# Kernel tuning notes

Hardware: AMD Instinct MI355X
Metric: run time of the kernel (lower is better)

## Reference

```python
import jax, jax.numpy as jnp
import numpy as np

NUM_BANDS, B, K, D = 5, 512, 64, 200
H = 4            # num attention heads
HID = 512        # selector hidden width
S = 0.02         # weight init scale


def setup_inputs() -> dict:
    key = jax.random.key(0)
    ks = jax.random.split(key, 8)
    F_IN = NUM_BANDS * K * D  # 64000
    return {
        "bands": jax.random.normal(ks[0], (NUM_BANDS, B, K, D), jnp.float32),
        "w1": jax.random.normal(ks[1], (HID, F_IN), jnp.float32) * S,
        "b1": jnp.zeros((HID,), jnp.float32),
        "w2": jax.random.normal(ks[2], (NUM_BANDS, HID), jnp.float32) * S,
        "b2": jnp.zeros((NUM_BANDS,), jnp.float32),
        "in_proj_w": jax.random.normal(ks[3], (3 * D, D), jnp.float32) * S,
        "in_proj_b": jnp.zeros((3 * D,), jnp.float32),
        "out_w": jax.random.normal(ks[4], (D, D), jnp.float32) * S,
        "out_b": jnp.zeros((D,), jnp.float32),
    }


def reference(bands, w1, b1, w2, b2, in_proj_w, in_proj_b, out_w, out_b):
    nb, Bb, k, d = bands.shape
    hd = d // H
    scale = 1.0 / np.sqrt(hd)

    # concat(bands, dim=1): [B, nb*k, d] in band-major order
    x = jnp.transpose(bands, (1, 0, 2, 3))           # [B, nb, k, d]
    kv_in = x.reshape(Bb, nb * k, d)                 # [B, nb*k, d]

    # router MLP + softmax + argmax band select
    flat = kv_in.reshape(Bb, -1)                     # [B, nb*k*d]
    h = jax.nn.relu(flat @ w1.T + b1)                # [B, HID]
    band_weights = jax.nn.softmax(h @ w2.T + b2, axis=-1)
    sel = jnp.argmax(band_weights, axis=-1)          # [B] int

    # gather selected band per sample as the query
    Q = bands[sel, jnp.arange(Bb)]                   # [B, k, d]

    # multihead cross-attention (torch nn.MultiheadAttention math)
    wq, wk, wv = jnp.split(in_proj_w, 3, axis=0)
    bq, bk, bv = jnp.split(in_proj_b, 3, axis=0)
    q = (Q @ wq.T + bq).reshape(Bb, k, H, hd).transpose(0, 2, 1, 3)        # [B,H,k,hd]
    kk = (kv_in @ wk.T + bk).reshape(Bb, nb * k, H, hd).transpose(0, 2, 1, 3)
    v = (kv_in @ wv.T + bv).reshape(Bb, nb * k, H, hd).transpose(0, 2, 1, 3)

    attn = jax.nn.softmax(jnp.einsum('bhqe,bhke->bhqk', q, kk) * scale, axis=-1)
    o = jnp.einsum('bhqk,bhke->bhqe', attn, v)       # [B,H,k,hd]
    o = o.transpose(0, 2, 1, 3).reshape(Bb, k, d)
    return o @ out_w.T + out_b                        # [B, k, d]
```

## Files before the change

### kernel.cpp

```cpp
#include <hip/hip_runtime.h>
#include <hip/hip_bf16.h>

#define NBANDS 5
#define BATCH  512
#define KQN    64
#define DM     200
#define NHEAD  4
#define HD     50
#define HIDW   512
#define TKV    320
#define FIN    64000
#define KSPLIT 20
#define KCH    3200
#define RCH    50
#define KPAD   232
#define NTT    13
#define KST    7
#define PLANE_ELEMS (KST * NTT * 64 * 8)

typedef __bf16  bf16x8 __attribute__((ext_vector_type(8)));
typedef float   f32x4  __attribute__((ext_vector_type(4)));

static __device__ inline unsigned short f2bf(float f) {
    __hip_bfloat16 h = __float2bfloat16(f);
    return *reinterpret_cast<unsigned short*>(&h);
}
static __device__ inline float bf2f(unsigned short u) {
    union { unsigned int i; float f; } x;
    x.i = ((unsigned int)u) << 16;
    return x.f;
}
static __device__ inline bf16x8 bf8zero() {
    union { bf16x8 v; unsigned int u[4]; } z;
    z.u[0] = z.u[1] = z.u[2] = z.u[3] = 0u;
    return z.v;
}
static __device__ inline void split8(const float4& a, const float4& b,
                                     bf16x8& hi, bf16x8& lo) {
    union { bf16x8 v; unsigned short u[8]; } H, L;
    const float xs[8] = {a.x, a.y, a.z, a.w, b.x, b.y, b.z, b.w};
#pragma unroll
    for (int i = 0; i < 8; ++i) {
        H.u[i] = f2bf(xs[i]);
        L.u[i] = f2bf(xs[i] - bf2f(H.u[i]));
    }
    hi = H.v; lo = L.v;
}

__global__ __launch_bounds__(256) void k_router_mfma(
    const float* __restrict__ bands, const float* __restrict__ w1,
    float* __restrict__ part)
{
    __shared__ __align__(16) unsigned short Ah[64][72];
    __shared__ __align__(16) unsigned short Al[64][72];
    __shared__ __align__(16) unsigned short Bh[64][72];
    __shared__ __align__(16) unsigned short Bl[64][72];

    const int lin     = (blockIdx.z << 6) + (blockIdx.y << 3) + blockIdx.x;
    const int logical = (lin & 7) * 160 + (lin >> 3);
    const int z   = logical >> 6;
    const int rem = logical & 63;
    const int j0  = (rem & 7) << 6;
    const int b0  = (rem >> 3) << 6;

    const int t  = threadIdx.x;
    const int w  = t >> 6, lane = t & 63;
    const int lm = lane & 15, quad = lane >> 4;
    const int m0 = w * 16;

    const int row0 = t >> 4, c4 = (t & 15) * 4;

    f32x4 acc[4];
#pragma unroll
    for (int nt = 0; nt < 4; ++nt) acc[nt] = (f32x4){0.f, 0.f, 0.f, 0.f};

    const int kbase = z * KCH;
    for (int chunk = 0; chunk < RCH; ++chunk) {
        const int kc = kbase + chunk * 64;
        const int band = kc / 12800;
        const float* abase = bands + (size_t)band * 6540800 + kc + c4;
        const float* bbase = w1 + (size_t)j0 * FIN + kc + c4;
        float4 av[4], bv[4];
#pragma unroll
        for (int r = 0; r < 4; ++r)
            av[r] = *(const float4*)(abase + (size_t)(b0 + row0 + r * 16) * 12800);
#pragma unroll
        for (int r = 0; r < 4; ++r)
            bv[r] = *(const float4*)(bbase + (size_t)(row0 + r * 16) * FIN);
        __syncthreads();
#pragma unroll
        for (int r = 0; r < 4; ++r) {
            const int row = row0 + r * 16;
            ushort4 hh, ll;
            hh.x = f2bf(av[r].x); ll.x = f2bf(av[r].x - bf2f(hh.x));
            hh.y = f2bf(av[r].y); ll.y = f2bf(av[r].y - bf2f(hh.y));
            hh.z = f2bf(av[r].z); ll.z = f2bf(av[r].z - bf2f(hh.z));
            hh.w = f2bf(av[r].w); ll.w = f2bf(av[r].w - bf2f(hh.w));
            *(ushort4*)&Ah[row][c4] = hh;
            *(ushort4*)&Al[row][c4] = ll;
        }
#pragma unroll
        for (int r = 0; r < 4; ++r) {
            const int row = row0 + r * 16;
            ushort4 hh, ll;
            hh.x = f2bf(bv[r].x); ll.x = f2bf(bv[r].x - bf2f(hh.x));
            hh.y = f2bf(bv[r].y); ll.y = f2bf(bv[r].y - bf2f(hh.y));
            hh.z = f2bf(bv[r].z); ll.z = f2bf(bv[r].z - bf2f(hh.z));
            hh.w = f2bf(bv[r].w); ll.w = f2bf(bv[r].w - bf2f(hh.w));
            *(ushort4*)&Bh[row][c4] = hh;
            *(ushort4*)&Bl[row][c4] = ll;
        }
        __syncthreads();
#pragma unroll
        for (int ks = 0; ks < 2; ++ks) {
            const int ka = ks * 32 + quad * 8;
            const bf16x8 a_h = *(const bf16x8*)&Ah[m0 + lm][ka];
            const bf16x8 a_l = *(const bf16x8*)&Al[m0 + lm][ka];
#pragma unroll
            for (int nt = 0; nt < 4; ++nt) {
                const bf16x8 b_h = *(const bf16x8*)&Bh[nt * 16 + lm][ka];
                const bf16x8 b_l = *(const bf16x8*)&Bl[nt * 16 + lm][ka];
                acc[nt] = __builtin_amdgcn_mfma_f32_16x16x32_bf16(a_h, b_h, acc[nt], 0, 0, 0);
                acc[nt] = __builtin_amdgcn_mfma_f32_16x16x32_bf16(a_l, b_h, acc[nt], 0, 0, 0);
                acc[nt] = __builtin_amdgcn_mfma_f32_16x16x32_bf16(a_h, b_l, acc[nt], 0, 0, 0);
            }
        }
    }
    float* po = part + (size_t)z * (BATCH * HIDW);
#pragma unroll
    for (int nt = 0; nt < 4; ++nt) {
        const int jj = j0 + nt * 16 + lm;
#pragma unroll
        for (int reg = 0; reg < 4; ++reg) {
            const int bb = b0 + m0 + quad * 4 + reg;
            po[(size_t)bb * HIDW + jj] = acc[nt][reg];
        }
    }
}

__global__ __launch_bounds__(256) void k_reduce_relu(
    const float* __restrict__ part, const float* __restrict__ b1,
    float* __restrict__ h)
{
    const int tid = blockIdx.x * 256 + threadIdx.x;
    float s = b1[tid & (HIDW - 1)];
#pragma unroll
    for (int z = 0; z < KSPLIT; ++z) s += part[z * (BATCH * HIDW) + tid];
    h[tid] = fmaxf(s, 0.f);
}

__global__ __launch_bounds__(256) void k_wprep(
    const float* __restrict__ ipw, unsigned short* __restrict__ Wb)
{
    const int j = blockIdx.x;
    const int c = threadIdx.x;
    if (c < KPAD) {
        const float v = (c < DM) ? ipw[(size_t)(DM + j) * DM + c] : 0.f;
        Wb[(size_t)j * KPAD + c] = f2bf(v);
    }
}

__global__ __launch_bounds__(256) void k_wpack(
    const float* __restrict__ ipw, const float* __restrict__ outw,
    unsigned short* __restrict__ WqHp, unsigned short* __restrict__ WqLp,
    unsigned short* __restrict__ OwHp, unsigned short* __restrict__ OwLp)
{
    const int p = blockIdx.x;
    const int ks = p / NTT, nt = p - ks * NTT;
    const int t = threadIdx.x;
    const int lane = t >> 2, e0 = (t & 3) * 2;
    const int lm = lane & 15, quad = lane >> 4;
    const int row = nt * 16 + lm;
    const int k  = ks * 32 + quad * 8 + e0;
    const float* src = (blockIdx.y == 0) ? ipw : outw;
    unsigned short* dh = (blockIdx.y == 0) ? WqHp : OwHp;
    unsigned short* dl = (blockIdx.y == 0) ? WqLp : OwLp;
    float v0 = 0.f, v1 = 0.f;
    if (row < DM && k < DM) {
        v0 = src[(size_t)row * DM + k];
        v1 = src[(size_t)row * DM + k + 1];
    }
    const int off = (p << 9) + (lane << 3) + e0;
    const unsigned short h0 = f2bf(v0), h1 = f2bf(v1);
    dh[off]     = h0;
    dh[off + 1] = h1;
    dl[off]     = f2bf(v0 - bf2f(h0));
    dl[off + 1] = f2bf(v1 - bf2f(h1));
}

__global__ __launch_bounds__(256) void k_argmax(
    const float* __restrict__ h, const float* __restrict__ w2,
    const float* __restrict__ b2, int* __restrict__ sel)
{
    __shared__ float red[NBANDS][256];
    const int b = blockIdx.x, t = threadIdx.x;
    float acc[NBANDS] = {0.f, 0.f, 0.f, 0.f, 0.f};
    for (int j = t; j < HIDW; j += 256) {
        const float hv = h[b * HIDW + j];
#pragma unroll
        for (int n = 0; n < NBANDS; ++n)
            acc[n] = fmaf(hv, w2[n * HIDW + j], acc[n]);
    }
#pragma unroll
    for (int n = 0; n < NBANDS; ++n) red[n][t] = acc[n];
    __syncthreads();
    for (int s = 128; s > 0; s >>= 1) {
        if (t < s) {
#pragma unroll
            for (int n = 0; n < NBANDS; ++n) red[n][t] += red[n][t + s];
        }
        __syncthreads();
    }
    if (t == 0) {
        int best = 0;
        float bv = red[0][0] + b2[0];
        for (int n = 1; n < NBANDS; ++n) {
            const float v = red[n][0] + b2[n];
            if (v > bv) { bv = v; best = n; }
        }
        sel[b] = best;
    }
}

template<bool BF16OUT>
static __device__ inline void proj_core(
    const float* __restrict__ x0,
    const unsigned short* __restrict__ Ph,
    const unsigned short* __restrict__ Pl,
    const float* __restrict__ bias,
    void* __restrict__ outp)
{
    const int t = threadIdx.x;
    const int w = t >> 6, lane = t & 63;
    const int lm = lane & 15, quad = lane >> 4;
    const int m0 = w * 16;
    const float* xrow = x0 + (size_t)(m0 + lm) * DM;

    f32x4 acc[NTT];
#pragma unroll
    for (int nt = 0; nt < NTT; ++nt) acc[nt] = (f32x4){0.f, 0.f, 0.f, 0.f};

#pragma unroll
    for (int ks = 0; ks < KST; ++ks) {
        const int k0 = ks * 32 + quad * 8;
        bf16x8 a_h = bf8zero(), a_l = bf8zero();
        if (k0 + 8 <= DM) {
            const float4 xa = *(const float4*)(xrow + k0);
            const float4 xb = *(const float4*)(xrow + k0 + 4);
            split8(xa, xb, a_h, a_l);
        }
        const unsigned short* ph = Ph + ((ks * NTT) << 9) + (lane << 3);
        const unsigned short* pl = Pl + ((ks * NTT) << 9) + (lane << 3);
#pragma unroll
        for (int nt = 0; nt < NTT; ++nt) {
            const bf16x8 b_h = *(const bf16x8*)(ph + (nt << 9));
            const bf16x8 b_l = *(const bf16x8*)(pl + (nt << 9));
            acc[nt] = __builtin_amdgcn_mfma_f32_16x16x32_bf16(a_h, b_h, acc[nt], 0, 0, 0);
            acc[nt] = __builtin_amdgcn_mfma_f32_16x16x32_bf16(a_l, b_h, acc[nt], 0, 0, 0);
            acc[nt] = __builtin_amdgcn_mfma_f32_16x16x32_bf16(a_h, b_l, acc[nt], 0, 0, 0);
        }
    }
#pragma unroll
    for (int nt = 0; nt < NTT; ++nt) {
        const int col = nt * 16 + lm;
        if (col < DM) {
            const float bs = bias[col];
#pragma unroll
            for (int reg = 0; reg < 4; ++reg) {
                const int row = m0 + quad * 4 + reg;
                const float v = acc[nt][reg] + bs;
                if (BF16OUT)
                    ((unsigned short*)outp)[(size_t)row * DM + col] = f2bf(v);
                else
                    ((float*)outp)[(size_t)row * DM + col] = v;
            }
        }
    }
}

__global__ __launch_bounds__(256) void k_qproj_mfma(
    const float* __restrict__ bands, const int* __restrict__ sel,
    const unsigned short* __restrict__ WqHp, const unsigned short* __restrict__ WqLp,
    const float* __restrict__ ipb, unsigned short* __restrict__ qb)
{
    const int b = blockIdx.x;
    const int band = sel[b];
    const float* x0 = bands + (size_t)((band * BATCH + b) * KQN) * DM;
    proj_core<true>(x0, WqHp, WqLp, ipb, qb + (size_t)(b * KQN) * DM);
}

__global__ __launch_bounds__(256) void k_outproj_mfma(
    const float* __restrict__ obuf, const unsigned short* __restrict__ OwHp,
    const unsigned short* __restrict__ OwLp, const float* __restrict__ outb,
    float* __restrict__ out)
{
    const int b = blockIdx.x;
    proj_core<false>(obuf + (size_t)(b * KQN) * DM, OwHp, OwLp, outb,
                     out + (size_t)(b * KQN) * DM);
}

__global__ __launch_bounds__(256) void k_kvproj(
    const float* __restrict__ bands, const unsigned short* __restrict__ Wb,
    const float* __restrict__ ipb, __hip_bfloat16* __restrict__ Kp,
    __hip_bfloat16* __restrict__ Vp)
{
    __shared__ __align__(16) unsigned short Xs[64][KPAD];
    __shared__ __align__(16) unsigned short Ws[80][KPAD];
    __shared__ float Bbias[80];
    const int t  = threadIdx.x;
    const int M0 = blockIdx.x * 64;
    const int n0 = blockIdx.y * 80;

    {
        const float4* wsrc = (const float4*)(Wb + (size_t)n0 * KPAD);
        float4* wdst = (float4*)&Ws[0][0];
        for (int i = t; i < 2320; i += 256) wdst[i] = wsrc[i];
    }
    if (t < 80) Bbias[t] = ipb[DM + n0 + t];
    for (int i = t; i < 64 * 50; i += 256) {
        const int r = i / 50, g = i - r * 50;
        const int gg = M0 + r;
        const int bb = gg / TKV, tk = gg - bb * TKV;
        const int band = tk >> 6, kk = tk & 63;
        const float4 x4 = *(const float4*)(bands
            + ((size_t)((band * BATCH + bb) * KQN + kk)) * DM + g * 4);
        ushort4 u;
        u.x = f2bf(x4.x); u.y = f2bf(x4.y); u.z = f2bf(x4.z); u.w = f2bf(x4.w);
        *(ushort4*)&Xs[r][g * 4] = u;
    }
    for (int i = t; i < 64 * 8; i += 256) {
        const int r = i >> 3, g = i & 7;
        ushort4 z; z.x = 0; z.y = 0; z.z = 0; z.w = 0;
        *(ushort4*)&Xs[r][DM + g * 4] = z;
    }
    __syncthreads();

    const int w = t >> 6, lane = t & 63;
    const int lm = lane & 15, quad = lane >> 4;
    const int m0 = w * 16;
    f32x4 acc[5];
#pragma unroll
    for (int nt = 0; nt < 5; ++nt) acc[nt] = (f32x4){0.f, 0.f, 0.f, 0.f};

#pragma unroll
    for (int ks = 0; ks < 7; ++ks) {
        const int ka = ks * 32 + quad * 8;
        const bf16x8 a = *(const bf16x8*)&Xs[m0 + lm][ka];
#pragma unroll
        for (int nt = 0; nt < 5; ++nt) {
            const bf16x8 bb8 = *(const bf16x8*)&Ws[nt * 16 + lm][ka];
            acc[nt] = __builtin_amdgcn_mfma_f32_16x16x32_bf16(a, bb8, acc[nt], 0, 0, 0);
        }
    }
#pragma unroll
    for (int nt = 0; nt < 5; ++nt) {
        const int col = n0 + nt * 16 + lm;
        const float bias = Bbias[nt * 16 + lm];
#pragma unroll
        for (int reg = 0; reg < 4; ++reg) {
            const int grow = M0 + m0 + quad * 4 + reg;
            const float v = acc[nt][reg] + bias;
            if (col < DM) Kp[(size_t)grow * DM + col] = __float2bfloat16(v);
            else          Vp[(size_t)grow * DM + (col - DM)] = __float2bfloat16(v);
        }
    }
}

__global__ __launch_bounds__(256) void k_attn(
    const unsigned short* __restrict__ qb, const __hip_bfloat16* __restrict__ Kp,
    const __hip_bfloat16* __restrict__ Vp, float* __restrict__ obuf)
{
    __shared__ __align__(16) unsigned short Qs[64][72];
    __shared__ __align__(16) unsigned short KP[320][72];
    __shared__ __align__(16) unsigned short Vt[64][328];
    __shared__ __align__(16) unsigned short Ps[64][328];
    const int b = blockIdx.x, hh = blockIdx.y;
    const int t = threadIdx.x;

    const unsigned short* qbase = qb + (size_t)(b * KQN) * DM + hh * HD;
    for (int idx = t; idx < 64 * 64; idx += 256) {
        const int r = idx >> 6, e = idx & 63;
        Qs[r][e] = (e < HD) ? qbase[(size_t)r * DM + e] : 0;
    }
    const unsigned short* kbase = (const unsigned short*)Kp + (size_t)b * TKV * DM + hh * HD;
    for (int idx = t; idx < 320 * 25; idx += 256) {
        const int key = idx / 25, g = idx - key * 25;
        *(unsigned int*)&KP[key][g * 2] =
            *(const unsigned int*)(kbase + (size_t)key * DM + g * 2);
    }
    for (int idx = t; idx < 320 * 7; idx += 256) {
        const int key = idx / 7, g = idx - key * 7;
        *(unsigned int*)&KP[key][50 + g * 2] = 0;
    }
    const unsigned short* vbase = (const unsigned short*)Vp + (size_t)b * TKV * DM + hh * HD;
    for (int idx = t; idx < 320 * 25; idx += 256) {
        const int key = idx / 25, g = idx - key * 25;
        const unsigned int v = *(const unsigned int*)(vbase + (size_t)key * DM + g * 2);
        Vt[g * 2][key]     = (unsigned short)(v & 0xffffu);
        Vt[g * 2 + 1][key] = (unsigned short)(v >> 16);
    }
    __syncthreads();

    const int w = t >> 6, lane = t & 63;
    const int lm = lane & 15, quad = lane >> 4;
    const int m0 = w * 16;

    f32x4 s[20];
#pragma unroll
    for (int nt = 0; nt < 20; ++nt) s[nt] = (f32x4){0.f, 0.f, 0.f, 0.f};
#pragma unroll
    for (int ks = 0; ks < 2; ++ks) {
        const int ka = ks * 32 + quad * 8;
        const bf16x8 a = *(const bf16x8*)&Qs[m0 + lm][ka];
#pragma unroll
        for (int nt = 0; nt < 20; ++nt) {
            const bf16x8 bb8 = *(const bf16x8*)&KP[nt * 16 + lm][ka];
            s[nt] = __builtin_amdgcn_mfma_f32_16x16x32_bf16(a, bb8, s[nt], 0, 0, 0);
        }
    }

    const float scale = 0.14142135623730951f;
    float inv[4];
#pragma unroll
    for (int reg = 0; reg < 4; ++reg) {
        float mx = -1e30f;
#pragma unroll
        for (int nt = 0; nt < 20; ++nt) {
            const float sv = s[nt][reg] * scale;
            s[nt][reg] = sv;
            mx = fmaxf(mx, sv);
        }
#pragma unroll
        for (int off = 1; off < 16; off <<= 1)
            mx = fmaxf(mx, __shfl_xor(mx, off, 64));
        float lsum = 0.f;
#pragma unroll
        for (int nt = 0; nt < 20; ++nt) {
            const float p = __expf(s[nt][reg] - mx);
            s[nt][reg] = p;
            lsum += p;
        }
#pragma unroll
        for (int off = 1; off < 16; off <<= 1)
            lsum += __shfl_xor(lsum, off, 64);
        inv[reg] = 1.f / lsum;
    }
#pragma unroll
    for (int reg = 0; reg < 4; ++reg) {
        const int row = m0 + quad * 4 + reg;
#pragma unroll
        for (int nt = 0; nt < 20; ++nt)
            Ps[row][nt * 16 + lm] = f2bf(s[nt][reg]);
    }
    __syncthreads();

    f32x4 o[4];
#pragma unroll
    for (int nt = 0; nt < 4; ++nt) o[nt] = (f32x4){0.f, 0.f, 0.f, 0.f};
#pragma unroll
    for (int ks = 0; ks < 10; ++ks) {
        const int ka = ks * 32 + quad * 8;
        const bf16x8 a = *(const bf16x8*)&Ps[m0 + lm][ka];
#pragma unroll
        for (int nt = 0; nt < 4; ++nt) {
            const bf16x8 bb8 = *(const bf16x8*)&Vt[nt * 16 + lm][ka];
            o[nt] = __builtin_amdgcn_mfma_f32_16x16x32_bf16(a, bb8, o[nt], 0, 0, 0);
        }
    }
    float* op = obuf + (size_t)(b * KQN) * DM + hh * HD;
#pragma unroll
    for (int nt = 0; nt < 4; ++nt) {
        const int e = nt * 16 + lm;
        if (e < HD) {
#pragma unroll
            for (int reg = 0; reg < 4; ++reg) {
                const int row = m0 + quad * 4 + reg;
                op[(size_t)row * DM + e] = o[nt][reg] * inv[reg];
            }
        }
    }
}

extern "C" void kernel_launch(void* const* d_in, const int* in_sizes, int n_in,
                              void* d_out, int out_size, void* d_ws, size_t ws_size,
                              hipStream_t stream)
{
    const float* bands = (const float*)d_in[0];
    const float* w1    = (const float*)d_in[1];
    const float* b1    = (const float*)d_in[2];
    const float* w2    = (const float*)d_in[3];
    const float* b2    = (const float*)d_in[4];
    const float* ipw   = (const float*)d_in[5];
    const float* ipb   = (const float*)d_in[6];
    const float* outw  = (const float*)d_in[7];
    const float* outb  = (const float*)d_in[8];
    float* out = (float*)d_out;

    if (ws_size < (size_t)192940032) return;

    char* ws = (char*)d_ws;
    int*   sel  = (int*)  (ws + 0);
    float* part = (float*)(ws + 4096);
    float* h    = (float*)(ws + 20975616);
    unsigned short* qb = (unsigned short*)(ws + 4096);
    unsigned short* Wb = (unsigned short*)(ws + 26218496);
    unsigned short* WqHp = (unsigned short*)(ws + 26404096);
    unsigned short* WqLp = (unsigned short*)(ws + 26497280);
    unsigned short* OwHp = (unsigned short*)(ws + 26590464);
    unsigned short* OwLp = (unsigned short*)(ws + 26683648);
    __hip_bfloat16* Kp = (__hip_bfloat16*)(ws + 26776832);
    __hip_bfloat16* Vp = (__hip_bfloat16*)(ws + 92312832);
    float* obuf = (float*)(ws + 157848832);

    k_wprep<<<400, 256, 0, stream>>>(ipw, Wb);
    k_wpack<<<dim3(KST * NTT, 2), 256, 0, stream>>>(ipw, outw, WqHp, WqLp, OwHp, OwLp);

    k_router_mfma<<<dim3(8, 8, KSPLIT), 256, 0, stream>>>(bands, w1, part);
    k_reduce_relu<<<(BATCH * HIDW) / 256, 256, 0, stream>>>(part, b1, h);
    k_argmax<<<BATCH, 256, 0, stream>>>(h, w2, b2, sel);
    k_qproj_mfma<<<BATCH, 256, 0, stream>>>(bands, sel, WqHp, WqLp, ipb, qb);
    k_kvproj<<<dim3(2560, 5), 256, 0, stream>>>(bands, Wb, ipb, Kp, Vp);
    k_attn<<<dim3(BATCH, NHEAD), 256, 0, stream>>>(qb, Kp, Vp, obuf);
    k_outproj_mfma<<<BATCH, 256, 0, stream>>>(obuf, OwHp, OwLp, outb, out);
}
```

Before: 935.7 us.

## Fuse K/V projection column tiles and feed MFMA from pre-packed global weights

The K/V projection kernel previously launched 5 column blocks per row tile, each re-reading and re-converting the same bands rows into LDS. It now computes all 400 K/V columns per block (25 accumulator tiles), loading each activation row straight from global into registers once. Weights are pre-packed into MFMA fragment order so they can be read directly from global/L2 without LDS staging or syncs. This cuts redundant reads of bands, at the cost of much higher register pressure (100 accumulator floats) and uncached global weight fetches per MFMA.

Result: no change. 941.9 us (+0.7%).

```diff
diff --git a/kernel.cpp b/kernel.cpp
--- a/kernel.cpp
+++ b/kernel.cpp
@@ -13,9 +13,9 @@
 #define KSPLIT 20
 #define KCH    3200
 #define RCH    50
-#define KPAD   232
 #define NTT    13
 #define KST    7
+#define NTKV   25
 #define PLANE_ELEMS (KST * NTT * 64 * 8)
 
 typedef __bf16  bf16x8 __attribute__((ext_vector_type(8)));
@@ -45,6 +45,13 @@
         L.u[i] = f2bf(xs[i] - bf2f(H.u[i]));
     }
     hi = H.v; lo = L.v;
+}
+static __device__ inline bf16x8 round8(const float4& a, const float4& b) {
+    union { bf16x8 v; unsigned short u[8]; } H;
+    const float xs[8] = {a.x, a.y, a.z, a.w, b.x, b.y, b.z, b.w};
+#pragma unroll
+    for (int i = 0; i < 8; ++i) H.u[i] = f2bf(xs[i]);
+    return H.v;
 }
 
 __global__ __launch_bounds__(256) void k_router_mfma(
@@ -147,17 +154,6 @@
 #pragma unroll
     for (int z = 0; z < KSPLIT; ++z) s += part[z * (BATCH * HIDW) + tid];
     h[tid] = fmaxf(s, 0.f);
-}
-
-__global__ __launch_bounds__(256) void k_wprep(
-    const float* __restrict__ ipw, unsigned short* __restrict__ Wb)
-{
-    const int j = blockIdx.x;
-    const int c = threadIdx.x;
-    if (c < KPAD) {
-        const float v = (c < DM) ? ipw[(size_t)(DM + j) * DM + c] : 0.f;
-        Wb[(size_t)j * KPAD + c] = f2bf(v);
-    }
 }
 
 __global__ __launch_bounds__(256) void k_wpack(
@@ -188,6 +184,26 @@
     dl[off + 1] = f2bf(v1 - bf2f(h1));
 }
 
+__global__ __launch_bounds__(256) void k_wpack_kv(
+    const float* __restrict__ ipw, unsigned short* __restrict__ Wkv)
+{
+    const int p = blockIdx.x;
+    const int ks = p / NTKV, nt = p - ks * NTKV;
+    const int t = threadIdx.x;
+    const int lane = t >> 2, e0 = (t & 3) * 2;
+    const int lm = lane & 15, quad = lane >> 4;
+    const int row = nt * 16 + lm;
+    const int k  = ks * 32 + quad * 8 + e0;
+    float v0 = 0.f, v1 = 0.f;
+    if (k < DM) {
+        v0 = ipw[(size_t)(DM + row) * DM + k];
+        v1 = ipw[(size_t)(DM + row) * DM + k + 1];
+    }
+    const int off = (p << 9) + (lane << 3) + e0;
+    Wkv[off]     = f2bf(v0);
+    Wkv[off + 1] = f2bf(v1);
+}
+
 __global__ __launch_bounds__(256) void k_argmax(
     const float* __restrict__ h, const float* __restrict__ w2,
     const float* __restrict__ b2, int* __restrict__ sel)
@@ -299,63 +315,46 @@
                      out + (size_t)(b * KQN) * DM);
 }
 
-__global__ __launch_bounds__(256) void k_kvproj(
-    const float* __restrict__ bands, const unsigned short* __restrict__ Wb,
+__global__ __launch_bounds__(256) void k_kvproj_pk(
+    const float* __restrict__ bands, const unsigned short* __restrict__ Wkv,
     const float* __restrict__ ipb, __hip_bfloat16* __restrict__ Kp,
     __hip_bfloat16* __restrict__ Vp)
 {
-    __shared__ __align__(16) unsigned short Xs[64][KPAD];
-    __shared__ __align__(16) unsigned short Ws[80][KPAD];
-    __shared__ float Bbias[80];
-    const int t  = threadIdx.x;
-    const int M0 = blockIdx.x * 64;
-    const int n0 = blockIdx.y * 80;
-
-    {
-        const float4* wsrc = (const float4*)(Wb + (size_t)n0 * KPAD);
-        float4* wdst = (float4*)&Ws[0][0];
-        for (int i = t; i < 2320; i += 256) wdst[i] = wsrc[i];
-    }
-    if (t < 80) Bbias[t] = ipb[DM + n0 + t];
-    for (int i = t; i < 64 * 50; i += 256) {
-        const int r = i / 50, g = i - r * 50;
-        const int gg = M0 + r;
-        const int bb = gg / TKV, tk = gg - bb * TKV;
-        const int band = tk >> 6, kk = tk & 63;
-        const float4 x4 = *(const float4*)(bands
-            + ((size_t)((band * BATCH + bb) * KQN + kk)) * DM + g * 4);
-        ushort4 u;
-        u.x = f2bf(x4.x); u.y = f2bf(x4.y); u.z = f2bf(x4.z); u.w = f2bf(x4.w);
-        *(ushort4*)&Xs[r][g * 4] = u;
-    }
-    for (int i = t; i < 64 * 8; i += 256) {
-        const int r = i >> 3, g = i & 7;
-        ushort4 z; z.x = 0; z.y = 0; z.z = 0; z.w = 0;
-        *(ushort4*)&Xs[r][DM + g * 4] = z;
-    }
-    __syncthreads();
-
+    const int t = threadIdx.x;
     const int w = t >> 6, lane = t & 63;
     const int lm = lane & 15, quad = lane >> 4;
     const int m0 = w * 16;
-    f32x4 acc[5];
-#pragma unroll
-    for (int nt = 0; nt < 5; ++nt) acc[nt] = (f32x4){0.f, 0.f, 0.f, 0.f};
-
-#pragma unroll
-    for (int ks = 0; ks < 7; ++ks) {
-        const int ka = ks * 32 + quad * 8;
-        const bf16x8 a = *(const bf16x8*)&Xs[m0 + lm][ka];
-#pragma unroll
-        for (int nt = 0; nt < 5; ++nt) {
-            const bf16x8 bb8 = *(const bf16x8*)&Ws[nt * 16 + lm][ka];
-            acc[nt] = __builtin_amdgcn_mfma_f32_16x16x32_bf16(a, bb8, acc[nt], 0, 0, 0);
-        }
-    }
-#pragma unroll
-    for (int nt = 0; nt < 5; ++nt) {
-        const int col = n0 + nt * 16 + lm;
-        const float bias = Bbias[nt * 16 + lm];
+    const int M0 = blockIdx.x * 64;
+
+    const int gg = M0 + m0 + lm;
+    const int bb = gg / TKV, tk = gg - bb * TKV;
+    const int band = tk >> 6, kk = tk & 63;
+    const float* xrow = bands + (size_t)((band * BATCH + bb) * KQN + kk) * DM;
+
+    f32x4 acc[NTKV];
+#pragma unroll
+    for (int nt = 0; nt < NTKV; ++nt) acc[nt] = (f32x4){0.f, 0.f, 0.f, 0.f};
+
+#pragma unroll
+    for (int ks = 0; ks < KST; ++ks) {
+        const int k0 = ks * 32 + quad * 8;
+        bf16x8 a = bf8zero();
+        if (k0 + 8 <= DM) {
+            const float4 xa = *(const float4*)(xrow + k0);
+            const float4 xb = *(const float4*)(xrow + k0 + 4);
+            a = round8(xa, xb);
+        }
+        const unsigned short* pb = Wkv + ((ks * NTKV) << 9) + (lane << 3);
+#pragma unroll
+        for (int nt = 0; nt < NTKV; ++nt) {
+            const bf16x8 b8 = *(const bf16x8*)(pb + (nt << 9));
+            acc[nt] = __builtin_amdgcn_mfma_f32_16x16x32_bf16(a, b8, acc[nt], 0, 0, 0);
+        }
+    }
+#pragma unroll
+    for (int nt = 0; nt < NTKV; ++nt) {
+        const int col = nt * 16 + lm;
+        const float bias = ipb[DM + col];
 #pragma unroll
         for (int reg = 0; reg < 4; ++reg) {
             const int grow = M0 + m0 + quad * 4 + reg;
@@ -503,7 +502,7 @@
     float* part = (float*)(ws + 4096);
     float* h    = (float*)(ws + 20975616);
     unsigned short* qb = (unsigned short*)(ws + 4096);
-    unsigned short* Wb = (unsigned short*)(ws + 26218496);
+    unsigned short* Wkv  = (unsigned short*)(ws + 26218496);
     unsigned short* WqHp = (unsigned short*)(ws + 26404096);
     unsigned short* WqLp = (unsigned short*)(ws + 26497280);
     unsigned short* OwHp = (unsigned short*)(ws + 26590464);
@@ -512,14 +511,14 @@
     __hip_bfloat16* Vp = (__hip_bfloat16*)(ws + 92312832);
     float* obuf = (float*)(ws + 157848832);
 
-    k_wprep<<<400, 256, 0, stream>>>(ipw, Wb);
+    k_wpack_kv<<<KST * NTKV, 256, 0, stream>>>(ipw, Wkv);
     k_wpack<<<dim3(KST * NTT, 2), 256, 0, stream>>>(ipw, outw, WqHp, WqLp, OwHp, OwLp);
 
     k_router_mfma<<<dim3(8, 8, KSPLIT), 256, 0, stream>>>(bands, w1, part);
     k_reduce_relu<<<(BATCH * HIDW) / 256, 256, 0, stream>>>(part, b1, h);
     k_argmax<<<BATCH, 256, 0, stream>>>(h, w2, b2, sel);
     k_qproj_mfma<<<BATCH, 256, 0, stream>>>(bands, sel, WqHp, WqLp, ipb, qb);
-    k_kvproj<<<dim3(2560, 5), 256, 0, stream>>>(bands, Wb, ipb, Kp, Vp);
+    k_kvproj_pk<<<2560, 256, 0, stream>>>(bands, Wkv, ipb, Kp, Vp);
     k_attn<<<dim3(BATCH, NHEAD), 256, 0, stream>>>(qb, Kp, Vp, obuf);
     k_outproj_mfma<<<BATCH, 256, 0, stream>>>(obuf, OwHp, OwLp, outb, out);
 }
```
